# Kernel optimization log

Hardware: AMD Instinct MI355X
Metric: run time of the kernel (lower is better)

The kernel has to match this reference:

```python
import jax, jax.numpy as jnp
import numpy as np

EPS = 1e-5
SLOPE = 0.2


def _edge_conv(x, w, gamma, beta, k):
    # x: (B,N,D); w: (O, 2D); returns (B,N,O)
    sq = jnp.sum(x * x, axis=-1)                                  # (B,N)
    # negative squared distance: larger = closer
    neg = 2.0 * jnp.einsum('bnd,bmd->bnm', x, x) - sq[:, :, None] - sq[:, None, :]
    _, idx = jax.lax.top_k(neg, k + 1)                            # (B,N,k+1)
    idx = idx[:, :, 1:]                                           # drop self -> (B,N,k)
    neigh = jax.vmap(lambda xb, ib: xb[ib])(x, idx)               # (B,N,k,D)
    ctr = jnp.broadcast_to(x[:, :, None, :], neigh.shape)
    edge = jnp.concatenate([neigh - ctr, ctr], axis=-1)           # (B,N,k,2D)
    h = jnp.einsum('bnkc,oc->bnko', edge, w)                      # 1x1 conv
    h = h * (gamma / jnp.sqrt(1.0 + EPS)) + beta                  # BN eval (mean=0,var=1)
    h = jnp.where(h > 0, h, SLOPE * h)                            # LeakyReLU(0.2)
    return jnp.max(h, axis=2)                                     # max over k -> (B,N,O)


def _bn_eval(x, gamma, beta):
    return x * (gamma / jnp.sqrt(1.0 + EPS)) + beta


def _lrelu(x):
    return jnp.where(x > 0, x, SLOPE * x)


def setup_inputs() -> dict:
    key = jax.random.key(0)
    ks = jax.random.split(key, 32)
    B, N, D, k, num_classes = 4, 4096, 3, 10, 3
    s = 0.1
    inp = {
        'points': jax.random.normal(ks[0], (B, N, D), jnp.float32),
        'k': k,
        'w1': jax.random.normal(ks[1], (64, 6), jnp.float32) * s,
        'g1': 1.0 + 0.1 * jax.random.normal(ks[2], (64,), jnp.float32),
        'b1': 0.1 * jax.random.normal(ks[3], (64,), jnp.float32),
        'w2': jax.random.normal(ks[4], (64, 128), jnp.float32) * s,
        'g2': 1.0 + 0.1 * jax.random.normal(ks[5], (64,), jnp.float32),
        'b2': 0.1 * jax.random.normal(ks[6], (64,), jnp.float32),
        'w3': jax.random.normal(ks[7], (128, 128), jnp.float32) * s,
        'g3': 1.0 + 0.1 * jax.random.normal(ks[8], (128,), jnp.float32),
        'b3': 0.1 * jax.random.normal(ks[9], (128,), jnp.float32),
        'w4': jax.random.normal(ks[10], (256, 256), jnp.float32) * s,
        'g4': 1.0 + 0.1 * jax.random.normal(ks[11], (256,), jnp.float32),
        'b4': 0.1 * jax.random.normal(ks[12], (256,), jnp.float32),
        'w5': jax.random.normal(ks[13], (1024, 512), jnp.float32) * s,
        'g5': 1.0 + 0.1 * jax.random.normal(ks[14], (1024,), jnp.float32),
        'b5': 0.1 * jax.random.normal(ks[15], (1024,), jnp.float32),
        'fw1': jax.random.normal(ks[16], (512, 1024), jnp.float32) * s,
        'fg1': 1.0 + 0.1 * jax.random.normal(ks[17], (512,), jnp.float32),
        'fbt1': 0.1 * jax.random.normal(ks[18], (512,), jnp.float32),
        'fw2': jax.random.normal(ks[19], (256, 512), jnp.float32) * s,
        'fb2': 0.1 * jax.random.normal(ks[20], (256,), jnp.float32),
        'fg2': 1.0 + 0.1 * jax.random.normal(ks[21], (256,), jnp.float32),
        'fbt2': 0.1 * jax.random.normal(ks[22], (256,), jnp.float32),
        'fw3': jax.random.normal(ks[23], (num_classes, 256), jnp.float32) * s,
        'fb3': 0.1 * jax.random.normal(ks[24], (num_classes,), jnp.float32),
    }
    return inp


def reference(points, w1, g1, b1, w2, g2, b2, w3, g3, b3, w4, g4, b4,
              w5, g5, b5, fw1, fg1, fbt1, fw2, fb2, fg2, fbt2, fw3, fb3, k):
    o1 = _edge_conv(points, w1, g1, b1, k)   # (B,N,64)
    o2 = _edge_conv(o1, w2, g2, b2, k)       # (B,N,64)
    o3 = _edge_conv(o2, w3, g3, b3, k)       # (B,N,128)
    o4 = _edge_conv(o3, w4, g4, b4, k)       # (B,N,256)
    cat = jnp.concatenate([o1, o2, o3, o4], axis=-1)   # (B,N,512)
    h = jnp.einsum('bnc,oc->bno', cat, w5)   # (B,N,1024)
    h = _lrelu(_bn_eval(h, g5, b5))
    h = jnp.max(h, axis=1)                   # global max over N -> (B,1024)
    # fc head (dropout = identity in eval)
    h = _lrelu(_bn_eval(h @ fw1.T, fg1, fbt1))
    h = _lrelu(_bn_eval(h @ fw2.T + fb2, fg2, fbt2))
    out = h @ fw3.T + fb3                    # (B,num_classes)
    return out
```

## Files before the change

kernel.cpp:

```cpp
#include <hip/hip_runtime.h>
#include <math.h>

#define N_PTS 4096
#define BATCH 4
#define KNN 10

__device__ __forceinline__ unsigned f2key(float x) {
    unsigned u = __float_as_uint(x);
    return (u & 0x80000000u) ? ~u : (u | 0x80000000u);
}
__device__ __forceinline__ float key2f(unsigned k) {
    unsigned u = (k & 0x80000000u) ? (k & 0x7FFFFFFFu) : ~k;
    return __uint_as_float(u);
}

__device__ __forceinline__ float lrelu(float h) { return (h > 0.f) ? h : 0.2f * h; }

__device__ __forceinline__ unsigned long long pack_kd(float v, int c) {
    return ((unsigned long long)f2key(v) << 32) | (unsigned)~(unsigned)c;
}

__device__ __forceinline__ unsigned long long bcast64(unsigned long long x, int src) {
    unsigned lo = (unsigned)__builtin_amdgcn_readlane((int)(unsigned)(x & 0xFFFFFFFFu), src);
    unsigned hi = (unsigned)__builtin_amdgcn_readlane((int)(unsigned)(x >> 32), src);
    return ((unsigned long long)hi << 32) | lo;
}

__global__ void sq_kernel(const float* __restrict__ x, int xstr, int D,
                          float* __restrict__ sq) {
    int g = blockIdx.x * blockDim.x + threadIdx.x;
    if (g >= BATCH * N_PTS) return;
    const float* row = x + (long)g * xstr;
    float s = 0.f;
    if ((D & 3) == 0) {
        for (int c = 0; c < D; c += 4) {
            float4 v = *(const float4*)&row[c];
            s += v.x * v.x + v.y * v.y + v.z * v.z + v.w * v.w;
        }
    } else {
        for (int c = 0; c < D; ++c) { float v = row[c]; s += v * v; }
    }
    sq[g] = s;
}

__global__ __launch_bounds__(256) void knn3_kernel(const float* __restrict__ x,
                                                   const float* __restrict__ sq,
                                                   int* __restrict__ idxout) {
    int b = blockIdx.y;
    int wave = threadIdx.x >> 6;
    int lane = threadIdx.x & 63;
    int row = blockIdx.x * 4 + wave;
    const float* xb = x + (long)b * N_PTS * 3;
    const float* sqb = sq + b * N_PTS;
    float x0 = xb[row * 3 + 0], x1 = xb[row * 3 + 1], x2 = xb[row * 3 + 2];
    float sr = sqb[row];

    unsigned long long elem = 0ull, T = 0ull;
    float Tf = -INFINITY;

    int c = lane;
    float y0 = xb[c * 3 + 0], y1 = xb[c * 3 + 1], y2 = xb[c * 3 + 2];
    float sc = sqb[c];
    for (int it = 0; it < 64; ++it) {
        float ny0, ny1, ny2, nsc;
        int nc = c + 64;
        if (it < 63) {
            ny0 = xb[nc * 3 + 0]; ny1 = xb[nc * 3 + 1]; ny2 = xb[nc * 3 + 2];
            nsc = sqb[nc];
        }
        float s = 0.f;
        s += x0 * y0; s += x1 * y1; s += x2 * y2;
        float d = 2.f * s - sr - sc;
        if (__ballot(d >= Tf)) {
            unsigned long long kq = pack_kd(d, c);
            unsigned long long mask;
            while ((mask = __ballot(kq > T)) != 0ull) {
                int src = __ffsll(mask) - 1;
                unsigned long long kb = bcast64(kq, src);
                if (lane == src) kq = 0ull;
                unsigned long long below = __ballot(elem > kb);
                int pos = __popcll(below);
                unsigned long long prev = __shfl_up(elem, 1);
                if (lane == pos) elem = kb;
                else if (lane > pos && lane <= 10) elem = prev;
                T = bcast64(elem, 10);
                Tf = key2f((unsigned)(T >> 32));
            }
        }
        y0 = ny0; y1 = ny1; y2 = ny2; sc = nsc; c = nc;
    }
    if (lane >= 1 && lane <= 10) {
        idxout[((long)b * N_PTS + row) * KNN + (lane - 1)] =
            (int)~(unsigned)(elem & 0xFFFFFFFFull);
    }
}

__global__ __launch_bounds__(256) void dist_kernel(const float* __restrict__ x,
                                                   const float* __restrict__ sq,
                                                   float* __restrict__ dist,
                                                   int xstr, int D, int row0) {
    __shared__ float As[16][132];
    __shared__ float Bs[16][132];
    int b = blockIdx.z;
    const float* xb = x + (long)b * N_PTS * xstr;
    const float* sqb = sq + b * N_PTS;
    float* db = dist + (long)b * 1024 * N_PTS;
    int r0 = row0 + blockIdx.y * 128;
    int c0 = blockIdx.x * 128;
    int tx = threadIdx.x & 15, ty = threadIdx.x >> 4;
    float acc[8][8] = {};
    int nk = (D + 15) >> 4;
    for (int kt = 0; kt < nk; ++kt) {
        int k0 = kt * 16;
        for (int e = threadIdx.x; e < 2048; e += 256) {
            int kk = e & 15, r = e >> 4;
            int c = k0 + kk;
            As[kk][r] = (c < D) ? xb[(long)(r0 + r) * xstr + c] : 0.f;
            Bs[kk][r] = (c < D) ? xb[(long)(c0 + r) * xstr + c] : 0.f;
        }
        __syncthreads();
        #pragma unroll
        for (int kk = 0; kk < 16; ++kk) {
            float a[8], bb[8];
            *(float4*)&a[0] = *(float4*)&As[kk][ty * 8];
            *(float4*)&a[4] = *(float4*)&As[kk][ty * 8 + 4];
            *(float4*)&bb[0] = *(float4*)&Bs[kk][tx * 8];
            *(float4*)&bb[4] = *(float4*)&Bs[kk][tx * 8 + 4];
            #pragma unroll
            for (int i = 0; i < 8; ++i)
                #pragma unroll
                for (int j = 0; j < 8; ++j) acc[i][j] += a[i] * bb[j];
        }
        __syncthreads();
    }
    #pragma unroll
    for (int i = 0; i < 8; ++i) {
        int lr = blockIdx.y * 128 + ty * 8 + i;
        float sr = sqb[r0 + ty * 8 + i];
        int cb = c0 + tx * 8;
        float4 v0, v1;
        v0.x = 2.f * acc[i][0] - sr - sqb[cb + 0];
        v0.y = 2.f * acc[i][1] - sr - sqb[cb + 1];
        v0.z = 2.f * acc[i][2] - sr - sqb[cb + 2];
        v0.w = 2.f * acc[i][3] - sr - sqb[cb + 3];
        v1.x = 2.f * acc[i][4] - sr - sqb[cb + 4];
        v1.y = 2.f * acc[i][5] - sr - sqb[cb + 5];
        v1.z = 2.f * acc[i][6] - sr - sqb[cb + 6];
        v1.w = 2.f * acc[i][7] - sr - sqb[cb + 7];
        *(float4*)&db[(long)lr * N_PTS + cb] = v0;
        *(float4*)&db[(long)lr * N_PTS + cb + 4] = v1;
    }
}

__global__ __launch_bounds__(256) void distsym_kernel(const float* __restrict__ x,
                                                      const float* __restrict__ sq,
                                                      float* __restrict__ dist,
                                                      int xstr, int D) {
    __shared__ float As[16][132];
    __shared__ float Bs[16][132];
    __shared__ float Tt[64][132];
    int b = blockIdx.z;
    int t = blockIdx.x, br = 0;
    while (t >= 32 - br) { t -= 32 - br; ++br; }
    int bc = br + t;
    const float* xb = x + (long)b * N_PTS * xstr;
    const float* sqb = sq + b * N_PTS;
    float* db = dist + (long)b * N_PTS * N_PTS;
    int r0 = br * 128, c0 = bc * 128;
    int tx = threadIdx.x & 15, ty = threadIdx.x >> 4;
    float acc[8][8] = {};
    int nk = (D + 15) >> 4;
    for (int kt = 0; kt < nk; ++kt) {
        int k0 = kt * 16;
        for (int e = threadIdx.x; e < 2048; e += 256) {
            int kk = e & 15, r = e >> 4;
            int c = k0 + kk;
            As[kk][r] = (c < D) ? xb[(long)(r0 + r) * xstr + c] : 0.f;
            Bs[kk][r] = (c < D) ? xb[(long)(c0 + r) * xstr + c] : 0.f;
        }
        __syncthreads();
        #pragma unroll
        for (int kk = 0; kk < 16; ++kk) {
            float a[8], bb[8];
            *(float4*)&a[0] = *(float4*)&As[kk][ty * 8];
            *(float4*)&a[4] = *(float4*)&As[kk][ty * 8 + 4];
            *(float4*)&bb[0] = *(float4*)&Bs[kk][tx * 8];
            *(float4*)&bb[4] = *(float4*)&Bs[kk][tx * 8 + 4];
            #pragma unroll
            for (int i = 0; i < 8; ++i)
                #pragma unroll
                for (int j = 0; j < 8; ++j) acc[i][j] += a[i] * bb[j];
        }
        __syncthreads();
    }
    float sqr[8], sqc[8];
    #pragma unroll
    for (int i = 0; i < 8; ++i) sqr[i] = sqb[r0 + ty * 8 + i];
    #pragma unroll
    for (int j = 0; j < 8; ++j) sqc[j] = sqb[c0 + tx * 8 + j];
    #pragma unroll
    for (int i = 0; i < 8; ++i) {
        int R = r0 + ty * 8 + i;
        int cb = c0 + tx * 8;
        float4 v0, v1;
        v0.x = 2.f * acc[i][0] - sqr[i] - sqc[0];
        v0.y = 2.f * acc[i][1] - sqr[i] - sqc[1];
        v0.z = 2.f * acc[i][2] - sqr[i] - sqc[2];
        v0.w = 2.f * acc[i][3] - sqr[i] - sqc[3];
        v1.x = 2.f * acc[i][4] - sqr[i] - sqc[4];
        v1.y = 2.f * acc[i][5] - sqr[i] - sqc[5];
        v1.z = 2.f * acc[i][6] - sqr[i] - sqc[6];
        v1.w = 2.f * acc[i][7] - sqr[i] - sqc[7];
        *(float4*)&db[(long)R * N_PTS + cb] = v0;
        *(float4*)&db[(long)R * N_PTS + cb + 4] = v1;
    }
    if (br == bc) return;
    #pragma unroll
    for (int h = 0; h < 2; ++h) {
        __syncthreads();
        if ((tx >> 3) == h) {
            int txl = tx & 7;
            #pragma unroll
            for (int j = 0; j < 8; ++j)
                #pragma unroll
                for (int i = 0; i < 8; ++i)
                    Tt[txl * 8 + j][ty * 8 + i] =
                        (2.f * acc[i][j] - sqc[j]) - sqr[i];
        }
        __syncthreads();
        for (int e = threadIdx.x; e < 2048; e += 256) {
            int rr = e >> 5, cc = (e & 31) << 2;
            *(float4*)&db[(long)(c0 + h * 64 + rr) * N_PTS + r0 + cc] =
                *(const float4*)&Tt[rr][cc];
        }
    }
}

__global__ __launch_bounds__(256) void topk_kernel(const float* __restrict__ dist,
                                                   int* __restrict__ idxout, int row0) {
    int b = blockIdx.y;
    int wave = threadIdx.x >> 6;
    int lane = threadIdx.x & 63;
    int row_local = blockIdx.x * 4 + wave;
    const float4* d4 =
        (const float4*)(dist + (long)b * 1024 * N_PTS + (long)row_local * N_PTS);

    unsigned long long elem = 0ull;
    unsigned long long T = 0ull;
    float Tf = -INFINITY;

    float4 cur = d4[lane];
    for (int jj = 0; jj < 16; ++jj) {
        float4 nxt;
        if (jj < 15) nxt = d4[(jj + 1) * 64 + lane];
        float vmax = fmaxf(fmaxf(cur.x, cur.y), fmaxf(cur.z, cur.w));
        if (__ballot(vmax >= Tf)) {
            int cbase = jj * 256 + lane * 4;
            unsigned long long kc[4];
            kc[0] = pack_kd(cur.x, cbase + 0);
            kc[1] = pack_kd(cur.y, cbase + 1);
            kc[2] = pack_kd(cur.z, cbase + 2);
            kc[3] = pack_kd(cur.w, cbase + 3);
            #pragma unroll
            for (int q = 0; q < 4; ++q) {
                unsigned long long kq = kc[q];
                unsigned long long mask;
                while ((mask = __ballot(kq > T)) != 0ull) {
                    int src = __ffsll(mask) - 1;
                    unsigned long long kb = bcast64(kq, src);
                    if (lane == src) kq = 0ull;
                    unsigned long long below = __ballot(elem > kb);
                    int pos = __popcll(below);
                    unsigned long long prev = __shfl_up(elem, 1);
                    if (lane == pos) elem = kb;
                    else if (lane > pos && lane <= 10) elem = prev;
                    T = bcast64(elem, 10);
                    Tf = key2f((unsigned)(T >> 32));
                }
            }
        }
        cur = nxt;
    }
    if (lane >= 1 && lane <= 10) {
        int c = (int)~(unsigned)(elem & 0xFFFFFFFFu);
        idxout[((long)b * N_PTS + row0 + row_local) * KNN + (lane - 1)] = c;
    }
}

__global__ __launch_bounds__(256) void topkfull_kernel(const float* __restrict__ dist,
                                                       int* __restrict__ idxout) {
    int b = blockIdx.y;
    int wave = threadIdx.x >> 6;
    int lane = threadIdx.x & 63;
    int row = blockIdx.x * 4 + wave;
    const float4* d4 =
        (const float4*)(dist + (long)b * N_PTS * N_PTS + (long)row * N_PTS);

    unsigned long long elem = 0ull;
    unsigned long long T = 0ull;
    float Tf = -INFINITY;

    float4 buf[4];
    #pragma unroll
    for (int p = 0; p < 4; ++p) buf[p] = d4[p * 64 + lane];
    for (int base = 0; base < 16; base += 4) {
        float4 nbuf[4];
        if (base + 4 < 16) {
            #pragma unroll
            for (int p = 0; p < 4; ++p) nbuf[p] = d4[(base + 4 + p) * 64 + lane];
        }
        #pragma unroll
        for (int p = 0; p < 4; ++p) {
            float4 cur = buf[p];
            float vmax = fmaxf(fmaxf(cur.x, cur.y), fmaxf(cur.z, cur.w));
            if (__ballot(vmax >= Tf)) {
                int cbase = (base + p) * 256 + lane * 4;
                unsigned long long kc[4];
                kc[0] = pack_kd(cur.x, cbase + 0);
                kc[1] = pack_kd(cur.y, cbase + 1);
                kc[2] = pack_kd(cur.z, cbase + 2);
                kc[3] = pack_kd(cur.w, cbase + 3);
                #pragma unroll
                for (int q = 0; q < 4; ++q) {
                    unsigned long long kq = kc[q];
                    unsigned long long mask;
                    while ((mask = __ballot(kq > T)) != 0ull) {
                        int src = __ffsll(mask) - 1;
                        unsigned long long kb = bcast64(kq, src);
                        if (lane == src) kq = 0ull;
                        unsigned long long below = __ballot(elem > kb);
                        int pos = __popcll(below);
                        unsigned long long prev = __shfl_up(elem, 1);
                        if (lane == pos) elem = kb;
                        else if (lane > pos && lane <= 10) elem = prev;
                        T = bcast64(elem, 10);
                        Tf = key2f((unsigned)(T >> 32));
                    }
                }
            }
        }
        #pragma unroll
        for (int p = 0; p < 4; ++p) buf[p] = nbuf[p];
    }
    if (lane >= 1 && lane <= 10) {
        int c = (int)~(unsigned)(elem & 0xFFFFFFFFu);
        idxout[((long)b * N_PTS + row) * KNN + (lane - 1)] = c;
    }
}

template <int DIN, int DOUT, int PTS, int TPP>
__global__ __launch_bounds__(256) void edgeconv_kernel(
    const float* __restrict__ x, int xstr, const int* __restrict__ idx,
    const float* __restrict__ w, const float* __restrict__ gamma,
    const float* __restrict__ beta, float* __restrict__ out, int outoff) {
    constexpr int DP = DIN + 1;
    constexpr int C2 = 2 * DIN;
    __shared__ float ctr[PTS][DP];
    __shared__ float nm[PTS][KNN][DP];
    int p0 = blockIdx.x * PTS;
    for (int e = threadIdx.x; e < PTS * DIN; e += 256) {
        int p = e / DIN, c = e - p * DIN;
        ctr[p][c] = x[(long)(p0 + p) * xstr + c];
    }
    __syncthreads();
    for (int e = threadIdx.x; e < PTS * KNN * DIN; e += 256) {
        int p = e / (KNN * DIN);
        int rem = e - p * (KNN * DIN);
        int kk = rem / DIN, c = rem - kk * DIN;
        int g = p0 + p;
        int nb = (g & ~(N_PTS - 1)) + idx[(long)g * KNN + kk];
        nm[p][kk][c] = x[(long)nb * xstr + c] - ctr[p][c];
    }
    __syncthreads();
    int p = threadIdx.x / TPP;
    int og = (threadIdx.x % TPP) * 4;
    float gs[4], bt[4];
    #pragma unroll
    for (int j = 0; j < 4; ++j) {
        gs[j] = gamma[og + j] / sqrtf(1.f + 1e-5f);
        bt[j] = beta[og + j];
    }
    float base[4] = {0.f, 0.f, 0.f, 0.f};
    for (int c = 0; c < DIN; ++c) {
        float cv = ctr[p][c];
        #pragma unroll
        for (int j = 0; j < 4; ++j) base[j] += cv * w[(og + j) * C2 + DIN + c];
    }
    float acc[KNN][4];
    #pragma unroll
    for (int kk = 0; kk < KNN; ++kk)
        #pragma unroll
        for (int j = 0; j < 4; ++j) acc[kk][j] = base[j];
    for (int c = 0; c < DIN; ++c) {
        float w4[4];
        #pragma unroll
        for (int j = 0; j < 4; ++j) w4[j] = w[(og + j) * C2 + c];
        #pragma unroll
        for (int kk = 0; kk < KNN; ++kk) {
            float nv = nm[p][kk][c];
            #pragma unroll
            for (int j = 0; j < 4; ++j) acc[kk][j] += nv * w4[j];
        }
    }
    float best[4] = {-INFINITY, -INFINITY, -INFINITY, -INFINITY};
    #pragma unroll
    for (int kk = 0; kk < KNN; ++kk)
        #pragma unroll
        for (int j = 0; j < 4; ++j)
            best[j] = fmaxf(best[j], lrelu(acc[kk][j] * gs[j] + bt[j]));
    #pragma unroll
    for (int j = 0; j < 4; ++j)
        out[(long)(p0 + p) * 512 + outoff + og + j] = best[j];
}

template <int DIN, int DOUT>
__global__ __launch_bounds__(256) void uvgemm_kernel(
    const float* __restrict__ x, int xoff, const float* __restrict__ w,
    float* __restrict__ uv) {
    constexpr int NC = 2 * DOUT;
    __shared__ float As[16][132];
    __shared__ float Bs[16][132];
    int r0 = blockIdx.y * 128;
    int c0 = blockIdx.x * 128;
    int tx = threadIdx.x & 15, ty = threadIdx.x >> 4;
    float acc[8][8] = {};
    #pragma unroll 1
    for (int kt = 0; kt < DIN / 16; ++kt) {
        int k0 = kt * 16;
        for (int e = threadIdx.x; e < 2048; e += 256) {
            int kk = e & 15, r = e >> 4;
            As[kk][r] = x[(long)(r0 + r) * 512 + xoff + k0 + kk];
            int jg = c0 + r;
            Bs[kk][r] = (jg < DOUT) ? w[(long)jg * (2 * DIN) + k0 + kk]
                                    : w[(long)(jg - DOUT) * (2 * DIN) + DIN + k0 + kk];
        }
        __syncthreads();
        #pragma unroll
        for (int kk = 0; kk < 16; ++kk) {
            float a[8], bb[8];
            *(float4*)&a[0] = *(float4*)&As[kk][ty * 8];
            *(float4*)&a[4] = *(float4*)&As[kk][ty * 8 + 4];
            *(float4*)&bb[0] = *(float4*)&Bs[kk][tx * 8];
            *(float4*)&bb[4] = *(float4*)&Bs[kk][tx * 8 + 4];
            #pragma unroll
            for (int i = 0; i < 8; ++i)
                #pragma unroll
                for (int j = 0; j < 8; ++j) acc[i][j] += a[i] * bb[j];
        }
        __syncthreads();
    }
    #pragma unroll
    for (int i = 0; i < 8; ++i) {
        int r = r0 + ty * 8 + i;
        int cb = c0 + tx * 8;
        *(float4*)&uv[(long)r * NC + cb] = *(float4*)&acc[i][0];
        *(float4*)&uv[(long)r * NC + cb + 4] = *(float4*)&acc[i][4];
    }
}

template <int DOUT>
__global__ __launch_bounds__(256) void edgemax_kernel(
    const float* __restrict__ uv, const int* __restrict__ idx,
    const float* __restrict__ gamma, const float* __restrict__ beta,
    float* __restrict__ out, int outoff) {
    constexpr int NC = 2 * DOUT;
    constexpr int TPP = DOUT / 4;
    constexpr int TP = 256 / TPP;
    __shared__ int sidx[TP][KNN];
    int p0 = blockIdx.x * TP;
    for (int e = threadIdx.x; e < TP * KNN; e += 256)
        sidx[e / KNN][e % KNN] = idx[(long)(p0 + e / KNN) * KNN + (e % KNN)];
    __syncthreads();
    int p = threadIdx.x / TPP;
    int og = (threadIdx.x % TPP) * 4;
    int g = p0 + p;
    int base_pt = g & ~(N_PTS - 1);
    const float* rowg = uv + (long)g * NC;
    float4 u_n = *(const float4*)&rowg[og];
    float4 v_n = *(const float4*)&rowg[DOUT + og];
    float c0 = v_n.x - u_n.x, c1 = v_n.y - u_n.y;
    float c2 = v_n.z - u_n.z, c3 = v_n.w - u_n.w;
    const float rs = 1.f / sqrtf(1.f + 1e-5f);
    float gs0 = gamma[og + 0] * rs, gs1 = gamma[og + 1] * rs;
    float gs2 = gamma[og + 2] * rs, gs3 = gamma[og + 3] * rs;
    float bt0 = beta[og + 0], bt1 = beta[og + 1];
    float bt2 = beta[og + 2], bt3 = beta[og + 3];
    float b0 = -INFINITY, b1 = -INFINITY, b2 = -INFINITY, b3 = -INFINITY;
    #pragma unroll
    for (int kk = 0; kk < KNN; ++kk) {
        int nb = base_pt + sidx[p][kk];
        float4 ub = *(const float4*)&uv[(long)nb * NC + og];
        b0 = fmaxf(b0, lrelu((ub.x + c0) * gs0 + bt0));
        b1 = fmaxf(b1, lrelu((ub.y + c1) * gs1 + bt1));
        b2 = fmaxf(b2, lrelu((ub.z + c2) * gs2 + bt2));
        b3 = fmaxf(b3, lrelu((ub.w + c3) * gs3 + bt3));
    }
    float4 o4; o4.x = b0; o4.y = b1; o4.z = b2; o4.w = b3;
    *(float4*)&out[(long)g * 512 + outoff + og] = o4;
}

__global__ void init_h5_kernel(unsigned* __restrict__ h5key) {
    int t = blockIdx.x * blockDim.x + threadIdx.x;
    if (t < BATCH * 1024) h5key[t] = 0u;
}

__global__ __launch_bounds__(256) void w5max_kernel(
    const float* __restrict__ cat, const float* __restrict__ w5,
    const float* __restrict__ g5, const float* __restrict__ b5,
    unsigned* __restrict__ h5key) {
    __shared__ float As[16][132];
    __shared__ float Bs[16][132];
    int b = blockIdx.z;
    int n0 = blockIdx.y * 128, o0 = blockIdx.x * 128;
    int tx = threadIdx.x & 15, ty = threadIdx.x >> 4;
    const float* A = cat + (long)b * N_PTS * 512;
    float acc[8][8] = {};
    for (int kt = 0; kt < 32; ++kt) {
        int k0 = kt * 16;
        for (int e = threadIdx.x; e < 2048; e += 256) {
            int kk = e & 15, r = e >> 4;
            As[kk][r] = A[(long)(n0 + r) * 512 + k0 + kk];
            Bs[kk][r] = w5[(long)(o0 + r) * 512 + k0 + kk];
        }
        __syncthreads();
        #pragma unroll
        for (int kk = 0; kk < 16; ++kk) {
            float a[8], bb[8];
            *(float4*)&a[0] = *(float4*)&As[kk][ty * 8];
            *(float4*)&a[4] = *(float4*)&As[kk][ty * 8 + 4];
            *(float4*)&bb[0] = *(float4*)&Bs[kk][tx * 8];
            *(float4*)&bb[4] = *(float4*)&Bs[kk][tx * 8 + 4];
            #pragma unroll
            for (int i = 0; i < 8; ++i)
                #pragma unroll
                for (int j = 0; j < 8; ++j) acc[i][j] += a[i] * bb[j];
        }
        __syncthreads();
    }
    float colmax[8];
    #pragma unroll
    for (int j = 0; j < 8; ++j) {
        int o = o0 + tx * 8 + j;
        float gsc = g5[o] / sqrtf(1.f + 1e-5f);
        float bto = b5[o];
        float m = -INFINITY;
        #pragma unroll
        for (int i = 0; i < 8; ++i)
            m = fmaxf(m, lrelu(acc[i][j] * gsc + bto));
        colmax[j] = m;
    }
    __syncthreads();
    float* red = &As[0][0];
    #pragma unroll
    for (int j = 0; j < 8; ++j) red[ty * 128 + tx * 8 + j] = colmax[j];
    __syncthreads();
    if (threadIdx.x < 128) {
        int col = threadIdx.x;
        float m = -INFINITY;
        #pragma unroll
        for (int t = 0; t < 16; ++t) m = fmaxf(m, red[t * 128 + col]);
        atomicMax(&h5key[b * 1024 + o0 + col], f2key(m));
    }
}

__global__ __launch_bounds__(256) void fchead_kernel(
    const unsigned* __restrict__ h5key,
    const float* __restrict__ fw1, const float* __restrict__ fg1,
    const float* __restrict__ fbt1,
    const float* __restrict__ fw2, const float* __restrict__ fb2,
    const float* __restrict__ fg2, const float* __restrict__ fbt2,
    const float* __restrict__ fw3, const float* __restrict__ fb3,
    float* __restrict__ out) {
    __shared__ float h5[1024];
    __shared__ float f1s[512];
    __shared__ float f2s[256];
    int b = blockIdx.x;
    int tid = threadIdx.x;
    for (int i = tid; i < 1024; i += 256) h5[i] = key2f(h5key[b * 1024 + i]);
    __syncthreads();
    for (int o = tid; o < 512; o += 256) {
        float s = 0.f;
        for (int c = 0; c < 1024; ++c) s += h5[c] * fw1[o * 1024 + c];
        float h = s * (fg1[o] / sqrtf(1.f + 1e-5f)) + fbt1[o];
        f1s[o] = lrelu(h);
    }
    __syncthreads();
    {
        int o = tid;
        float s = fb2[o];
        for (int c = 0; c < 512; ++c) s += f1s[c] * fw2[o * 512 + c];
        float h = s * (fg2[o] / sqrtf(1.f + 1e-5f)) + fbt2[o];
        f2s[o] = lrelu(h);
    }
    __syncthreads();
    if (tid < 3) {
        int o = tid;
        float s = fb3[o];
        for (int c = 0; c < 256; ++c) s += f2s[c] * fw3[o * 256 + c];
        out[b * 3 + o] = s;
    }
}

extern "C" void kernel_launch(void* const* d_in, const int* in_sizes, int n_in,
                              void* d_out, int out_size, void* d_ws, size_t ws_size,
                              hipStream_t stream) {
    const float* points = (const float*)d_in[0];
    const float* w1 = (const float*)d_in[2];
    const float* g1 = (const float*)d_in[3];
    const float* b1 = (const float*)d_in[4];
    const float* w2 = (const float*)d_in[5];
    const float* g2 = (const float*)d_in[6];
    const float* b2 = (const float*)d_in[7];
    const float* w3 = (const float*)d_in[8];
    const float* g3 = (const float*)d_in[9];
    const float* b3 = (const float*)d_in[10];
    const float* w4 = (const float*)d_in[11];
    const float* g4 = (const float*)d_in[12];
    const float* b4 = (const float*)d_in[13];
    const float* w5 = (const float*)d_in[14];
    const float* g5 = (const float*)d_in[15];
    const float* b5 = (const float*)d_in[16];
    const float* fw1 = (const float*)d_in[17];
    const float* fg1 = (const float*)d_in[18];
    const float* fbt1 = (const float*)d_in[19];
    const float* fw2 = (const float*)d_in[20];
    const float* fb2 = (const float*)d_in[21];
    const float* fg2 = (const float*)d_in[22];
    const float* fbt2 = (const float*)d_in[23];
    const float* fw3 = (const float*)d_in[24];
    const float* fb3 = (const float*)d_in[25];

    float* ws = (float*)d_ws;
    float* cat = ws;
    float* sq = cat + (long)BATCH * N_PTS * 512;
    unsigned* h5key = (unsigned*)(sq + BATCH * N_PTS);
    float* f1 = (float*)(h5key + BATCH * 1024);
    float* f2 = f1 + BATCH * 512;
    int* idxbuf = (int*)(f2 + BATCH * 256);
    float* dist = (float*)(idxbuf + (long)BATCH * N_PTS * KNN);
    float* uv = dist;

    size_t need = (size_t)((char*)(dist + (size_t)BATCH * N_PTS * N_PTS) -
                           (char*)d_ws);
    bool fullp = ws_size >= need;

    auto knn = [&](const float* xbase, int xstr, int D) {
        sq_kernel<<<64, 256, 0, stream>>>(xbase, xstr, D, sq);
        if (fullp) {
            distsym_kernel<<<dim3(528, 1, BATCH), 256, 0, stream>>>(
                xbase, sq, dist, xstr, D);
            topkfull_kernel<<<dim3(N_PTS / 4, BATCH), 256, 0, stream>>>(dist, idxbuf);
        } else {
            for (int r0 = 0; r0 < N_PTS; r0 += 1024) {
                dist_kernel<<<dim3(32, 8, BATCH), 256, 0, stream>>>(xbase, sq, dist,
                                                                    xstr, D, r0);
                topk_kernel<<<dim3(256, BATCH), 256, 0, stream>>>(dist, idxbuf, r0);
            }
        }
    };

    sq_kernel<<<64, 256, 0, stream>>>(points, 3, 3, sq);
    knn3_kernel<<<dim3(N_PTS / 4, BATCH), 256, 0, stream>>>(points, sq, idxbuf);
    edgeconv_kernel<3, 64, 16, 16><<<N_PTS * BATCH / 16, 256, 0, stream>>>(
        points, 3, idxbuf, w1, g1, b1, cat, 0);

    knn(cat + 0, 512, 64);
    uvgemm_kernel<64, 64><<<dim3(1, 128), 256, 0, stream>>>(cat, 0, w2, uv);
    edgemax_kernel<64><<<1024, 256, 0, stream>>>(uv, idxbuf, g2, b2, cat, 64);

    knn(cat + 64, 512, 64);
    uvgemm_kernel<64, 128><<<dim3(2, 128), 256, 0, stream>>>(cat, 64, w3, uv);
    edgemax_kernel<128><<<2048, 256, 0, stream>>>(uv, idxbuf, g3, b3, cat, 128);

    knn(cat + 128, 512, 128);
    uvgemm_kernel<128, 256><<<dim3(4, 128), 256, 0, stream>>>(cat, 128, w4, uv);
    edgemax_kernel<256><<<4096, 256, 0, stream>>>(uv, idxbuf, g4, b4, cat, 256);

    init_h5_kernel<<<16, 256, 0, stream>>>(h5key);
    w5max_kernel<<<dim3(8, 32, BATCH), 256, 0, stream>>>(cat, w5, g5, b5, h5key);

    fchead_kernel<<<BATCH, 256, 0, stream>>>(h5key, fw1, fg1, fbt1, fw2, fb2,
                                             fg2, fbt2, fw3, fb3, (float*)d_out);
}
```

Baseline: 1.734 ms.

## Record per-tile row maxima in distance kernel and prune top-k scan

The symmetric distance kernel now also writes the maximum of each 128-column tile for every row into a small side buffer. The top-k kernel no longer streams the full 4096-wide row. It repeatedly picks the tile with the highest recorded max, loads only that tile, and stops once no remaining tile max can beat the current 10th-best threshold. This cuts the global reads in top-k, since most tiles are never loaded. In exchange it adds reductions and extra stores to the distance kernel, needs a larger workspace, and turns top-k into a serial loop over tiles whose length depends on the data.

```diff
diff --git a/kernel.cpp b/kernel.cpp
--- a/kernel.cpp
+++ b/kernel.cpp
@@ -155,6 +155,7 @@
 __global__ __launch_bounds__(256) void distsym_kernel(const float* __restrict__ x,
                                                       const float* __restrict__ sq,
                                                       float* __restrict__ dist,
+                                                      float* __restrict__ maxbuf,
                                                       int xstr, int D) {
     __shared__ float As[16][132];
     __shared__ float Bs[16][132];
@@ -213,6 +214,12 @@
         v1.w = 2.f * acc[i][7] - sqr[i] - sqc[7];
         *(float4*)&db[(long)R * N_PTS + cb] = v0;
         *(float4*)&db[(long)R * N_PTS + cb + 4] = v1;
+        float tm = fmaxf(fmaxf(fmaxf(v0.x, v0.y), fmaxf(v0.z, v0.w)),
+                         fmaxf(fmaxf(v1.x, v1.y), fmaxf(v1.z, v1.w)));
+        #pragma unroll
+        for (int off = 1; off < 16; off <<= 1)
+            tm = fmaxf(tm, __shfl_xor(tm, off, 16));
+        if (tx == 0) maxbuf[((long)b * N_PTS + R) * 32 + bc] = tm;
     }
     if (br == bc) return;
     #pragma unroll
@@ -232,6 +239,16 @@
             int rr = e >> 5, cc = (e & 31) << 2;
             *(float4*)&db[(long)(c0 + h * 64 + rr) * N_PTS + r0 + cc] =
                 *(const float4*)&Tt[rr][cc];
+        }
+        {
+            int rr = threadIdx.x >> 2, q = threadIdx.x & 3;
+            float tm = -INFINITY;
+            #pragma unroll
+            for (int cc = 0; cc < 32; ++cc) tm = fmaxf(tm, Tt[rr][q * 32 + cc]);
+            tm = fmaxf(tm, __shfl_xor(tm, 1, 4));
+            tm = fmaxf(tm, __shfl_xor(tm, 2, 4));
+            if (q == 0)
+                maxbuf[((long)b * N_PTS + c0 + h * 64 + rr) * 32 + br] = tm;
         }
     }
 }
@@ -287,60 +304,51 @@
     }
 }
 
-__global__ __launch_bounds__(256) void topkfull_kernel(const float* __restrict__ dist,
-                                                       int* __restrict__ idxout) {
+__global__ __launch_bounds__(256) void topkms_kernel(const float* __restrict__ dist,
+                                                     const float* __restrict__ maxbuf,
+                                                     int* __restrict__ idxout) {
     int b = blockIdx.y;
     int wave = threadIdx.x >> 6;
     int lane = threadIdx.x & 63;
     int row = blockIdx.x * 4 + wave;
-    const float4* d4 =
-        (const float4*)(dist + (long)b * N_PTS * N_PTS + (long)row * N_PTS);
-
-    unsigned long long elem = 0ull;
-    unsigned long long T = 0ull;
+    const float* drow = dist + (long)b * N_PTS * N_PTS + (long)row * N_PTS;
+    float mx = (lane < 32) ? maxbuf[((long)b * N_PTS + row) * 32 + lane] : -INFINITY;
+
+    unsigned long long elem = 0ull, T = 0ull;
     float Tf = -INFINITY;
 
-    float4 buf[4];
-    #pragma unroll
-    for (int p = 0; p < 4; ++p) buf[p] = d4[p * 64 + lane];
-    for (int base = 0; base < 16; base += 4) {
-        float4 nbuf[4];
-        if (base + 4 < 16) {
-            #pragma unroll
-            for (int p = 0; p < 4; ++p) nbuf[p] = d4[(base + 4 + p) * 64 + lane];
-        }
-        #pragma unroll
-        for (int p = 0; p < 4; ++p) {
-            float4 cur = buf[p];
-            float vmax = fmaxf(fmaxf(cur.x, cur.y), fmaxf(cur.z, cur.w));
-            if (__ballot(vmax >= Tf)) {
-                int cbase = (base + p) * 256 + lane * 4;
-                unsigned long long kc[4];
-                kc[0] = pack_kd(cur.x, cbase + 0);
-                kc[1] = pack_kd(cur.y, cbase + 1);
-                kc[2] = pack_kd(cur.z, cbase + 2);
-                kc[3] = pack_kd(cur.w, cbase + 3);
-                #pragma unroll
-                for (int q = 0; q < 4; ++q) {
-                    unsigned long long kq = kc[q];
-                    unsigned long long mask;
-                    while ((mask = __ballot(kq > T)) != 0ull) {
-                        int src = __ffsll(mask) - 1;
-                        unsigned long long kb = bcast64(kq, src);
-                        if (lane == src) kq = 0ull;
-                        unsigned long long below = __ballot(elem > kb);
-                        int pos = __popcll(below);
-                        unsigned long long prev = __shfl_up(elem, 1);
-                        if (lane == pos) elem = kb;
-                        else if (lane > pos && lane <= 10) elem = prev;
-                        T = bcast64(elem, 10);
-                        Tf = key2f((unsigned)(T >> 32));
-                    }
-                }
+    while (1) {
+        float bv = mx; int bi = lane;
+        #pragma unroll
+        for (int off = 32; off > 0; off >>= 1) {
+            float ov = __shfl_xor(bv, off);
+            int oi = __shfl_xor(bi, off);
+            if (ov > bv || (ov == bv && oi < bi)) { bv = ov; bi = oi; }
+        }
+        if (!(bv >= Tf)) break;
+        int cb = bi * 128 + lane * 2;
+        float2 v = *(const float2*)&drow[cb];
+        unsigned long long kc[2];
+        kc[0] = pack_kd(v.x, cb);
+        kc[1] = pack_kd(v.y, cb + 1);
+        #pragma unroll
+        for (int q = 0; q < 2; ++q) {
+            unsigned long long kq = kc[q];
+            unsigned long long mask;
+            while ((mask = __ballot(kq > T)) != 0ull) {
+                int src = __ffsll(mask) - 1;
+                unsigned long long kb = bcast64(kq, src);
+                if (lane == src) kq = 0ull;
+                unsigned long long below = __ballot(elem > kb);
+                int pos = __popcll(below);
+                unsigned long long prev = __shfl_up(elem, 1);
+                if (lane == pos) elem = kb;
+                else if (lane > pos && lane <= 10) elem = prev;
+                T = bcast64(elem, 10);
+                Tf = key2f((unsigned)(T >> 32));
             }
         }
-        #pragma unroll
-        for (int p = 0; p < 4; ++p) buf[p] = nbuf[p];
+        if (lane == bi) mx = -INFINITY;
     }
     if (lane >= 1 && lane <= 10) {
         int c = (int)~(unsigned)(elem & 0xFFFFFFFFu);
@@ -639,8 +647,9 @@
     int* idxbuf = (int*)(f2 + BATCH * 256);
     float* dist = (float*)(idxbuf + (long)BATCH * N_PTS * KNN);
     float* uv = dist;
-
-    size_t need = (size_t)((char*)(dist + (size_t)BATCH * N_PTS * N_PTS) -
+    float* maxbuf = dist + (size_t)BATCH * N_PTS * N_PTS;
+
+    size_t need = (size_t)((char*)(maxbuf + (size_t)BATCH * N_PTS * 32) -
                            (char*)d_ws);
     bool fullp = ws_size >= need;
 
@@ -648,8 +657,9 @@
         sq_kernel<<<64, 256, 0, stream>>>(xbase, xstr, D, sq);
         if (fullp) {
             distsym_kernel<<<dim3(528, 1, BATCH), 256, 0, stream>>>(
-                xbase, sq, dist, xstr, D);
-            topkfull_kernel<<<dim3(N_PTS / 4, BATCH), 256, 0, stream>>>(dist, idxbuf);
+                xbase, sq, dist, maxbuf, xstr, D);
+            topkms_kernel<<<dim3(N_PTS / 4, BATCH), 256, 0, stream>>>(dist, maxbuf,
+                                                                      idxbuf);
         } else {
             for (int r0 = 0; r0 < N_PTS; r0 += 1024) {
                 dist_kernel<<<dim3(32, 8, BATCH), 256, 0, stream>>>(xbase, sq, dist,
```

New measurement: 1.735 ms. Within noise of the previous version (+0.0%).
